# Optimization experiments

Measured on AMD Instinct MI355X. Metric: run time of the kernel, lower is better.

## Reference

```python
import jax, jax.numpy as jnp
import numpy as np

B, T, D, F, E, K = 2, 1024, 1024, 2048, 8, 2

def setup_inputs() -> dict:
    key = jax.random.key(0)
    ks = jax.random.split(key, 9)
    s = 0.02
    return {
        "states": jax.random.normal(ks[0], (B, T, D), dtype=jnp.float32),
        "Wg": jax.random.normal(ks[1], (D, E), dtype=jnp.float32) * s,
        "W_in": jax.random.normal(ks[2], (E, D, F), dtype=jnp.float32) * s,
        "b_in": jnp.zeros((E, F), dtype=jnp.float32),
        "W_scale": jax.random.normal(ks[3], (E, D, F), dtype=jnp.float32) * s,
        "b_scale": jnp.zeros((E, F), dtype=jnp.float32),
        "W_out": jax.random.normal(ks[4], (E, F, D), dtype=jnp.float32) * s,
        "b_out": jnp.zeros((E, D), dtype=jnp.float32),
        "num_selected": K,
    }

def reference(states, Wg, W_in, b_in, W_scale, b_scale, W_out, b_out, num_selected):
    b, t, d = states.shape
    x = states.reshape(-1, d)                      # [N, D]
    n = x.shape[0]
    # router: softmax over experts, then top-k + renormalize
    probs = jax.nn.softmax(x @ Wg, axis=-1)        # [N, E]
    topw, topi = jax.lax.top_k(probs, num_selected)  # [N, K]
    topw = topw / topw.sum(axis=-1, keepdims=True)
    # dense combine weights [N, E]: zero except selected experts
    w_full = jnp.zeros_like(probs).at[jnp.arange(n)[:, None], topi].set(topw)
    # gated-GELU expert MLPs, batched over experts
    h = jnp.einsum('nd,edf->enf', x, W_in) + b_in[:, None, :]       # [E, N, F]
    s = jnp.einsum('nd,edf->enf', x, W_scale) + b_scale[:, None, :]
    inner = jax.nn.gelu(h, approximate=False) * s                    # exact GELU (torch default)
    y = jnp.einsum('enf,efd->end', inner, W_out) + b_out[:, None, :]  # [E, N, D]
    out = jnp.einsum('end,ne->nd', y, w_full)                         # weighted combine
    return out.reshape(b, t, d)
```

## Files before the change

kernel.cpp:

```cpp
#include <hip/hip_runtime.h>
#include <hip/hip_bf16.h>
#include <math.h>

#define N_TOK 2048
#define DIM   1024
#define FF    2048
#define NEXP  8
#define NSLOT (N_TOK * 2)

typedef __attribute__((ext_vector_type(8))) short short8;
typedef __attribute__((ext_vector_type(4))) float f32x4;
typedef _Float16 half_t;
typedef __attribute__((ext_vector_type(4))) _Float16 h16x4;

__device__ __forceinline__ unsigned short f2bf(float f) {
    unsigned int u = __float_as_uint(f);
    u += 0x7FFFu + ((u >> 16) & 1u);
    return (unsigned short)(u >> 16);
}

#define GLOAD_LDS16(g, l) \
    __builtin_amdgcn_global_load_lds((const __attribute__((address_space(1))) unsigned int*)(g), \
                                     (__attribute__((address_space(3))) unsigned int*)(l), 16, 0, 0)

__global__ __launch_bounds__(256) void k_router(const float* __restrict__ x,
        const float* __restrict__ Wg, int* __restrict__ hdr,
        int* __restrict__ tok_e, float* __restrict__ tok_w) {
    int wave = threadIdx.x >> 6, lane = threadIdx.x & 63;
    int t = blockIdx.x * 4 + wave;
    float acc[NEXP];
#pragma unroll
    for (int e = 0; e < NEXP; ++e) acc[e] = 0.f;
    const float* xr = x + (size_t)t * DIM;
    for (int d = lane; d < DIM; d += 64) {
        float xv = xr[d];
        const float* wr = Wg + d * NEXP;
#pragma unroll
        for (int e = 0; e < NEXP; ++e) acc[e] += xv * wr[e];
    }
#pragma unroll
    for (int off = 32; off > 0; off >>= 1) {
#pragma unroll
        for (int e = 0; e < NEXP; ++e) acc[e] += __shfl_down(acc[e], off);
    }
    if (lane == 0) {
        int e0 = 0;
#pragma unroll
        for (int e = 1; e < NEXP; ++e) if (acc[e] > acc[e0]) e0 = e;
        int e1 = -1;
#pragma unroll
        for (int e = 0; e < NEXP; ++e) {
            if (e == e0) continue;
            if (e1 < 0 || acc[e] > acc[e1]) e1 = e;
        }
        float w0 = 1.f / (1.f + expf(acc[e1] - acc[e0]));
        tok_e[2 * t] = e0; tok_e[2 * t + 1] = e1;
        tok_w[2 * t] = w0; tok_w[2 * t + 1] = 1.f - w0;
        atomicAdd(&hdr[e0], 1);
        atomicAdd(&hdr[e1], 1);
    }
}

__global__ void k_scan(int* hdr) {
    if (threadIdx.x == 0 && blockIdx.x == 0) {
        int s = 0;
        for (int e = 0; e < NEXP; ++e) {
            hdr[16 + e] = s;
            hdr[8 + e]  = s;
            s += hdr[e];
        }
        hdr[24] = s;
    }
}

__global__ __launch_bounds__(256) void k_assign(const float* __restrict__ x,
        int* __restrict__ hdr, const int* __restrict__ tok_e,
        int* __restrict__ tok_slot, unsigned short* __restrict__ xg) {
    __shared__ int sh[2];
    int t = blockIdx.x;
    if (threadIdx.x == 0) {
        int e0 = tok_e[2 * t], e1 = tok_e[2 * t + 1];
        int p0 = atomicAdd(&hdr[8 + e0], 1);
        int p1 = atomicAdd(&hdr[8 + e1], 1);
        tok_slot[2 * t] = p0; tok_slot[2 * t + 1] = p1;
        sh[0] = p0; sh[1] = p1;
    }
    __syncthreads();
    int s0 = sh[0], s1 = sh[1];
    const float4* xr = (const float4*)(x + (size_t)t * DIM);
    float4 v = xr[threadIdx.x];
    ushort4 b;
    b.x = f2bf(v.x); b.y = f2bf(v.y); b.z = f2bf(v.z); b.w = f2bf(v.w);
    ((ushort4*)(xg + (size_t)s0 * DIM))[threadIdx.x] = b;
    ((ushort4*)(xg + (size_t)s1 * DIM))[threadIdx.x] = b;
}

__global__ __launch_bounds__(256) void k_cvt(
        const float* __restrict__ s0, const float* __restrict__ s1,
        const float* __restrict__ s2, unsigned short* __restrict__ d0,
        unsigned short* __restrict__ d1, unsigned short* __restrict__ d2) {
    int bz = blockIdx.y;
    int which = bz >> 3, e = bz & 7;
    int R = (which == 2) ? FF : DIM;
    int C = (which == 2) ? DIM : FF;
    const float* S = ((which == 0) ? s0 : (which == 1) ? s1 : s2) + (size_t)e * DIM * FF;
    unsigned short* D = ((which == 0) ? d0 : (which == 1) ? d1 : d2) + (size_t)e * DIM * FF;
    int tilesx = C >> 6;
    int tx = blockIdx.x % tilesx, ty = blockIdx.x / tilesx;
    int c0 = tx * 64, r0 = ty * 128;
    __shared__ unsigned short sh[64][132];
    int t = threadIdx.x;
    int rl = t >> 4, cl = (t & 15) * 4;
#pragma unroll
    for (int p = 0; p < 8; ++p) {
        int r = p * 16 + rl;
        float4 v = *(const float4*)(S + (size_t)(r0 + r) * C + c0 + cl);
        sh[cl + 0][r] = f2bf(v.x);
        sh[cl + 1][r] = f2bf(v.y);
        sh[cl + 2][r] = f2bf(v.z);
        sh[cl + 3][r] = f2bf(v.w);
    }
    __syncthreads();
    int ol = t >> 4, wl = (t & 15) * 8;
#pragma unroll
    for (int p = 0; p < 4; ++p) {
        int oc = p * 16 + ol;
        uint2 lo = *(const uint2*)&sh[oc][wl];
        uint2 hi = *(const uint2*)&sh[oc][wl + 4];
        uint4 v = make_uint4(lo.x, lo.y, hi.x, hi.y);
        *(uint4*)(D + (size_t)(c0 + oc) * R + r0 + wl) = v;
    }
}

__global__ __launch_bounds__(256, 4) void k_expert_hs(
        const unsigned short* __restrict__ xg,
        const unsigned short* __restrict__ Wth,
        const unsigned short* __restrict__ Wts,
        const float* __restrict__ b_in, const float* __restrict__ b_sc,
        const int* __restrict__ hdr, unsigned short* __restrict__ inner) {
    int e = blockIdx.z;
    int cnt = hdr[e];
    int mtile = blockIdx.y;
    if (mtile * 128 >= cnt) return;
    int base = hdr[16 + e];
    int f0 = blockIdx.x * 64;

    __shared__ unsigned short As[2 * 128 * 32];
    __shared__ unsigned short Bh[2 * 64 * 32];
    __shared__ unsigned short Bs[2 * 64 * 32];

    int tid = threadIdx.x;
    int wave = tid >> 6, lane = tid & 63;
    int lr = lane & 15, lq = lane >> 4;
    int wm = (wave >> 1) * 64, wf = (wave & 1) * 32;

    f32x4 acch[4][2], accs[4][2];
#pragma unroll
    for (int mi = 0; mi < 4; ++mi)
#pragma unroll
        for (int fi = 0; fi < 2; ++fi) {
            acch[mi][fi] = (f32x4){0.f, 0.f, 0.f, 0.f};
            accs[mi][fi] = (f32x4){0.f, 0.f, 0.f, 0.f};
        }

    int swzc = (lane & 3) ^ ((lane >> 3) & 3);
    int goff = (lane >> 2) * DIM + swzc * 8;
    int rdo = lr * 32 + (lq ^ ((lr >> 1) & 3)) * 8;

    const unsigned short* Abase = xg  + (size_t)(base + mtile * 128) * DIM + goff;
    const unsigned short* Hbase = Wth + ((size_t)e * FF + f0) * DIM + goff;
    const unsigned short* Sbase = Wts + ((size_t)e * FF + f0) * DIM + goff;
    int pa0 = wave * 16, pa1 = 64 + wave * 16, pb = wave * 16;

    GLOAD_LDS16(Abase + (size_t)pa0 * DIM, &As[pa0 * 32]);
    GLOAD_LDS16(Abase + (size_t)pa1 * DIM, &As[pa1 * 32]);
    GLOAD_LDS16(Hbase + (size_t)pb * DIM, &Bh[pb * 32]);
    GLOAD_LDS16(Sbase + (size_t)pb * DIM, &Bs[pb * 32]);
    __syncthreads();

    const int NSTEP = DIM / 32;
    for (int t = 0; t < NSTEP; ++t) {
        int coA = (t & 1) * (128 * 32), coB = (t & 1) * (64 * 32);
        if (t + 1 < NSTEP) {
            int noA = ((t & 1) ^ 1) * (128 * 32), noB = ((t & 1) ^ 1) * (64 * 32);
            int k1 = (t + 1) * 32;
            GLOAD_LDS16(Abase + (size_t)pa0 * DIM + k1, &As[noA + pa0 * 32]);
            GLOAD_LDS16(Abase + (size_t)pa1 * DIM + k1, &As[noA + pa1 * 32]);
            GLOAD_LDS16(Hbase + (size_t)pb * DIM + k1, &Bh[noB + pb * 32]);
            GLOAD_LDS16(Sbase + (size_t)pb * DIM + k1, &Bs[noB + pb * 32]);
        }

        short8 af[4], bhf[2], bsf[2];
#pragma unroll
        for (int mi = 0; mi < 4; ++mi)
            af[mi] = *(const short8*)&As[coA + (wm + mi * 16) * 32 + rdo];
#pragma unroll
        for (int fi = 0; fi < 2; ++fi) {
            bhf[fi] = *(const short8*)&Bh[coB + (wf + fi * 16) * 32 + rdo];
            bsf[fi] = *(const short8*)&Bs[coB + (wf + fi * 16) * 32 + rdo];
        }
#pragma unroll
        for (int mi = 0; mi < 4; ++mi)
#pragma unroll
            for (int fi = 0; fi < 2; ++fi) {
                acch[mi][fi] = __builtin_amdgcn_mfma_f32_16x16x32_bf16(
                    af[mi], bhf[fi], acch[mi][fi], 0, 0, 0);
                accs[mi][fi] = __builtin_amdgcn_mfma_f32_16x16x32_bf16(
                    af[mi], bsf[fi], accs[mi][fi], 0, 0, 0);
            }
        __syncthreads();
    }

#pragma unroll
    for (int fi = 0; fi < 2; ++fi) {
        int f = f0 + wf + fi * 16 + lr;
        float bi = b_in[e * FF + f];
        float bs2 = b_sc[e * FF + f];
#pragma unroll
        for (int mi = 0; mi < 4; ++mi) {
#pragma unroll
            for (int r = 0; r < 4; ++r) {
                int rl = wm + mi * 16 + lq * 4 + r;
                int grow = mtile * 128 + rl;
                if (grow < cnt) {
                    float h = acch[mi][fi][r] + bi;
                    float s = accs[mi][fi][r] + bs2;
                    float g = 0.5f * h * (1.f + erff(h * 0.70710678f));
                    inner[(size_t)(base + grow) * FF + f] = f2bf(g * s);
                }
            }
        }
    }
}

__global__ __launch_bounds__(256, 4) void k_expert_out(
        const unsigned short* __restrict__ inner,
        const unsigned short* __restrict__ Wto,
        const int* __restrict__ hdr, half_t* __restrict__ pbuf) {
    int e = blockIdx.z & 7;
    int ks = blockIdx.z >> 3;
    int cnt = hdr[e];
    int mtile = blockIdx.y;
    if (mtile * 128 >= cnt) return;
    int base = hdr[16 + e];
    int d0 = blockIdx.x * 128;

    __shared__ unsigned short As[2 * 128 * 32];
    __shared__ unsigned short Bt[2 * 128 * 32];

    int tid = threadIdx.x;
    int wave = tid >> 6, lane = tid & 63;
    int lr = lane & 15, lq = lane >> 4;
    int wm = (wave >> 1) * 64, wn = (wave & 1) * 64;

    f32x4 acc[4][4];
#pragma unroll
    for (int mi = 0; mi < 4; ++mi)
#pragma unroll
        for (int ni = 0; ni < 4; ++ni) acc[mi][ni] = (f32x4){0.f, 0.f, 0.f, 0.f};

    int swzc = (lane & 3) ^ ((lane >> 3) & 3);
    int goff = (lane >> 2) * FF + swzc * 8;
    int rdo = lr * 32 + (lq ^ ((lr >> 1) & 3)) * 8;

    const unsigned short* Abase = inner + (size_t)(base + mtile * 128) * FF + goff;
    const unsigned short* Bbase = Wto + ((size_t)e * DIM + d0) * FF + goff;
    int pa0 = wave * 16, pa1 = 64 + wave * 16;

    int kbeg = ks * (FF / 2);

    GLOAD_LDS16(Abase + (size_t)pa0 * FF + kbeg, &As[pa0 * 32]);
    GLOAD_LDS16(Abase + (size_t)pa1 * FF + kbeg, &As[pa1 * 32]);
    GLOAD_LDS16(Bbase + (size_t)pa0 * FF + kbeg, &Bt[pa0 * 32]);
    GLOAD_LDS16(Bbase + (size_t)pa1 * FF + kbeg, &Bt[pa1 * 32]);
    __syncthreads();

    const int NSTEP = (FF / 2) / 32;
    for (int t = 0; t < NSTEP; ++t) {
        int co = (t & 1) * (128 * 32);
        if (t + 1 < NSTEP) {
            int no = ((t & 1) ^ 1) * (128 * 32);
            int k1 = kbeg + (t + 1) * 32;
            GLOAD_LDS16(Abase + (size_t)pa0 * FF + k1, &As[no + pa0 * 32]);
            GLOAD_LDS16(Abase + (size_t)pa1 * FF + k1, &As[no + pa1 * 32]);
            GLOAD_LDS16(Bbase + (size_t)pa0 * FF + k1, &Bt[no + pa0 * 32]);
            GLOAD_LDS16(Bbase + (size_t)pa1 * FF + k1, &Bt[no + pa1 * 32]);
        }

        short8 af[4], bfm[4];
#pragma unroll
        for (int mi = 0; mi < 4; ++mi)
            af[mi] = *(const short8*)&As[co + (wm + mi * 16) * 32 + rdo];
#pragma unroll
        for (int ni = 0; ni < 4; ++ni)
            bfm[ni] = *(const short8*)&Bt[co + (wn + ni * 16) * 32 + rdo];
#pragma unroll
        for (int mi = 0; mi < 4; ++mi)
#pragma unroll
            for (int ni = 0; ni < 4; ++ni)
                acc[mi][ni] = __builtin_amdgcn_mfma_f32_16x16x32_bf16(
                    af[mi], bfm[ni], acc[mi][ni], 0, 0, 0);
        __syncthreads();
    }

    half_t* P = pbuf + (size_t)ks * NSLOT * DIM;
#pragma unroll
    for (int ni = 0; ni < 4; ++ni) {
        int d = d0 + wn + ni * 16 + lr;
#pragma unroll
        for (int mi = 0; mi < 4; ++mi) {
#pragma unroll
            for (int r = 0; r < 4; ++r) {
                int rl = wm + mi * 16 + lq * 4 + r;
                int grow = mtile * 128 + rl;
                if (grow < cnt)
                    P[(size_t)(base + grow) * DIM + d] = (half_t)acc[mi][ni][r];
            }
        }
    }
}

__global__ __launch_bounds__(256) void k_combine(const half_t* __restrict__ pbuf,
        const int* __restrict__ tok_slot, const int* __restrict__ tok_e,
        const float* __restrict__ tok_w, const float* __restrict__ b_out,
        float* __restrict__ out) {
    int t = blockIdx.x;
    int d = threadIdx.x * 4;
    int s0 = tok_slot[2 * t], s1 = tok_slot[2 * t + 1];
    int e0 = tok_e[2 * t], e1 = tok_e[2 * t + 1];
    float w0 = tok_w[2 * t], w1 = tok_w[2 * t + 1];
    const half_t* pA = pbuf;
    const half_t* pB = pbuf + (size_t)NSLOT * DIM;
    h16x4 a0 = *(const h16x4*)&pA[(size_t)s0 * DIM + d];
    h16x4 a1 = *(const h16x4*)&pB[(size_t)s0 * DIM + d];
    h16x4 c0 = *(const h16x4*)&pA[(size_t)s1 * DIM + d];
    h16x4 c1 = *(const h16x4*)&pB[(size_t)s1 * DIM + d];
    float4 b0 = *(const float4*)&b_out[e0 * DIM + d];
    float4 b1 = *(const float4*)&b_out[e1 * DIM + d];
    float4 r;
    r.x = w0 * ((float)a0.x + (float)a1.x + b0.x) + w1 * ((float)c0.x + (float)c1.x + b1.x);
    r.y = w0 * ((float)a0.y + (float)a1.y + b0.y) + w1 * ((float)c0.y + (float)c1.y + b1.y);
    r.z = w0 * ((float)a0.z + (float)a1.z + b0.z) + w1 * ((float)c0.z + (float)c1.z + b1.z);
    r.w = w0 * ((float)a0.w + (float)a1.w + b0.w) + w1 * ((float)c0.w + (float)c1.w + b1.w);
    *(float4*)&out[(size_t)t * DIM + d] = r;
}

extern "C" void kernel_launch(void* const* d_in, const int* in_sizes, int n_in,
                              void* d_out, int out_size, void* d_ws, size_t ws_size,
                              hipStream_t stream) {
    (void)in_sizes; (void)n_in; (void)out_size; (void)ws_size;
    const float* x    = (const float*)d_in[0];
    const float* Wg   = (const float*)d_in[1];
    const float* Win  = (const float*)d_in[2];
    const float* b_in = (const float*)d_in[3];
    const float* Wsc  = (const float*)d_in[4];
    const float* b_sc = (const float*)d_in[5];
    const float* Wout = (const float*)d_in[6];
    const float* b_out= (const float*)d_in[7];
    float* out = (float*)d_out;

    char* ws = (char*)d_ws;
    int*   hdr      = (int*)ws;
    int*   tok_e    = (int*)(ws + 256);
    float* tok_w    = (float*)(ws + 16640);
    int*   tok_slot = (int*)(ws + 33024);
    unsigned short* xg    = (unsigned short*)(ws + 65792);
    unsigned short* inner = (unsigned short*)(ws + 65792 + 8388608);
    half_t* pbuf = (half_t*)(ws + 65792 + 8388608 + 16777216);
    unsigned short* wt_h = (unsigned short*)(ws + 65792 + 8388608 + 16777216 + 16777216);
    unsigned short* wt_s = wt_h + (size_t)NEXP * FF * DIM;
    unsigned short* wt_o = wt_s + (size_t)NEXP * FF * DIM;

    hipMemsetAsync(hdr, 0, 256, stream);
    k_cvt<<<dim3(256, 24), dim3(256), 0, stream>>>(Win, Wsc, Wout, wt_h, wt_s, wt_o);
    k_router<<<dim3(N_TOK / 4), dim3(256), 0, stream>>>(x, Wg, hdr, tok_e, tok_w);
    k_scan<<<dim3(1), dim3(64), 0, stream>>>(hdr);
    k_assign<<<dim3(N_TOK), dim3(256), 0, stream>>>(x, hdr, tok_e, tok_slot, xg);
    k_expert_hs<<<dim3(FF / 64, 16, NEXP), dim3(256), 0, stream>>>(xg, wt_h, wt_s, b_in, b_sc, hdr, inner);
    k_expert_out<<<dim3(DIM / 128, 16, NEXP * 2), dim3(256), 0, stream>>>(inner, wt_o, hdr, pbuf);
    k_combine<<<dim3(N_TOK), dim3(256), 0, stream>>>(pbuf, tok_slot, tok_e, tok_w, b_out, out);
}
```

Baseline: 446.0 us.

## Fuse weight conversion, routing and token scatter into one prep kernel

Merges the weight transpose/convert kernel, the router, the scan and the token assignment into a single launch. When the workspace is large enough, each expert gets a fixed slab of N_TOK slots, so the router can assign slots with atomics directly and scatter bf16 token rows itself, dropping the scan and assign launches. The conversion tiles are also enlarged to 256 rows per block. This removes launches and serialization between small kernels, at the cost of a much larger workspace and sparser slot layout, and it falls back to the old path when the workspace is small.

Measured after the change: 437.3 us. 2.0% less time.

```diff
diff --git a/kernel.cpp b/kernel.cpp
--- a/kernel.cpp
+++ b/kernel.cpp
@@ -7,6 +7,7 @@
 #define FF    2048
 #define NEXP  8
 #define NSLOT (N_TOK * 2)
+#define NCVT  3072
 
 typedef __attribute__((ext_vector_type(8))) short short8;
 typedef __attribute__((ext_vector_type(4))) float f32x4;
@@ -23,15 +24,64 @@
     __builtin_amdgcn_global_load_lds((const __attribute__((address_space(1))) unsigned int*)(g), \
                                      (__attribute__((address_space(3))) unsigned int*)(l), 16, 0, 0)
 
-__global__ __launch_bounds__(256) void k_router(const float* __restrict__ x,
-        const float* __restrict__ Wg, int* __restrict__ hdr,
-        int* __restrict__ tok_e, float* __restrict__ tok_w) {
-    int wave = threadIdx.x >> 6, lane = threadIdx.x & 63;
-    int t = blockIdx.x * 4 + wave;
+__global__ __launch_bounds__(256) void k_prep(
+        const float* __restrict__ x, const float* __restrict__ Wg,
+        const float* __restrict__ Win, const float* __restrict__ Wsc,
+        const float* __restrict__ Wout,
+        unsigned short* __restrict__ wt_h, unsigned short* __restrict__ wt_s,
+        unsigned short* __restrict__ wt_o,
+        int* __restrict__ hdr, int* __restrict__ tok_e,
+        float* __restrict__ tok_w, int* __restrict__ tok_slot,
+        unsigned short* __restrict__ xg, int mode) {
+    __shared__ unsigned short sh[64][260];
+    int gid = blockIdx.x;
+    int t = threadIdx.x;
+
+    if (gid < NCVT) {
+        int bz = gid >> 7;
+        int which = bz >> 3, e = bz & 7;
+        int R = (which == 2) ? FF : DIM;
+        int C = (which == 2) ? DIM : FF;
+        const float* S = ((which == 0) ? Win : (which == 1) ? Wsc : Wout)
+                         + (size_t)e * DIM * FF;
+        unsigned short* D = ((which == 0) ? wt_h : (which == 1) ? wt_s : wt_o)
+                            + (size_t)e * DIM * FF;
+        int local = gid & 127;
+        int tilesx = C >> 6;
+        int tx = local % tilesx, ty = local / tilesx;
+        int c0 = tx * 64, r0 = ty * 256;
+        int rl = t >> 4, cl = (t & 15) * 4;
+#pragma unroll
+        for (int p = 0; p < 16; ++p) {
+            int r = p * 16 + rl;
+            float4 v = *(const float4*)(S + (size_t)(r0 + r) * C + c0 + cl);
+            sh[cl + 0][r] = f2bf(v.x);
+            sh[cl + 1][r] = f2bf(v.y);
+            sh[cl + 2][r] = f2bf(v.z);
+            sh[cl + 3][r] = f2bf(v.w);
+        }
+        __syncthreads();
+        int ol = t >> 5, wl = (t & 31) * 8;
+#pragma unroll
+        for (int q = 0; q < 8; ++q) {
+            int oc = q * 8 + ol;
+            uint2 lo = *(const uint2*)&sh[oc][wl];
+            uint2 hi = *(const uint2*)&sh[oc][wl + 4];
+            *(uint4*)(D + (size_t)(c0 + oc) * R + r0 + wl) =
+                make_uint4(lo.x, lo.y, hi.x, hi.y);
+        }
+        return;
+    }
+
+    int rblk = gid - NCVT;
+    int wave = t >> 6, lane = t & 63;
+    int tok = rblk * 4 + wave;
+    if (mode && gid == NCVT && t < NEXP) hdr[16 + t] = t * N_TOK;
+
     float acc[NEXP];
 #pragma unroll
     for (int e = 0; e < NEXP; ++e) acc[e] = 0.f;
-    const float* xr = x + (size_t)t * DIM;
+    const float* xr = x + (size_t)tok * DIM;
     for (int d = lane; d < DIM; d += 64) {
         float xv = xr[d];
         const float* wr = Wg + d * NEXP;
@@ -43,6 +93,7 @@
 #pragma unroll
         for (int e = 0; e < NEXP; ++e) acc[e] += __shfl_down(acc[e], off);
     }
+    int s0 = 0, s1 = 0;
     if (lane == 0) {
         int e0 = 0;
 #pragma unroll
@@ -54,10 +105,29 @@
             if (e1 < 0 || acc[e] > acc[e1]) e1 = e;
         }
         float w0 = 1.f / (1.f + expf(acc[e1] - acc[e0]));
-        tok_e[2 * t] = e0; tok_e[2 * t + 1] = e1;
-        tok_w[2 * t] = w0; tok_w[2 * t + 1] = 1.f - w0;
-        atomicAdd(&hdr[e0], 1);
-        atomicAdd(&hdr[e1], 1);
+        tok_e[2 * tok] = e0; tok_e[2 * tok + 1] = e1;
+        tok_w[2 * tok] = w0; tok_w[2 * tok + 1] = 1.f - w0;
+        if (mode) {
+            int p0 = atomicAdd(&hdr[e0], 1);
+            int p1 = atomicAdd(&hdr[e1], 1);
+            s0 = e0 * N_TOK + p0; s1 = e1 * N_TOK + p1;
+            tok_slot[2 * tok] = s0; tok_slot[2 * tok + 1] = s1;
+        } else {
+            atomicAdd(&hdr[e0], 1);
+            atomicAdd(&hdr[e1], 1);
+        }
+    }
+    if (mode) {
+        s0 = __shfl(s0, 0); s1 = __shfl(s1, 0);
+        const float4* xv4 = (const float4*)xr;
+#pragma unroll
+        for (int j = 0; j < 4; ++j) {
+            float4 v = xv4[lane + j * 64];
+            ushort4 b;
+            b.x = f2bf(v.x); b.y = f2bf(v.y); b.z = f2bf(v.z); b.w = f2bf(v.w);
+            ((ushort4*)(xg + (size_t)s0 * DIM))[lane + j * 64] = b;
+            ((ushort4*)(xg + (size_t)s1 * DIM))[lane + j * 64] = b;
+        }
     }
 }
 
@@ -93,43 +163,6 @@
     b.x = f2bf(v.x); b.y = f2bf(v.y); b.z = f2bf(v.z); b.w = f2bf(v.w);
     ((ushort4*)(xg + (size_t)s0 * DIM))[threadIdx.x] = b;
     ((ushort4*)(xg + (size_t)s1 * DIM))[threadIdx.x] = b;
-}
-
-__global__ __launch_bounds__(256) void k_cvt(
-        const float* __restrict__ s0, const float* __restrict__ s1,
-        const float* __restrict__ s2, unsigned short* __restrict__ d0,
-        unsigned short* __restrict__ d1, unsigned short* __restrict__ d2) {
-    int bz = blockIdx.y;
-    int which = bz >> 3, e = bz & 7;
-    int R = (which == 2) ? FF : DIM;
-    int C = (which == 2) ? DIM : FF;
-    const float* S = ((which == 0) ? s0 : (which == 1) ? s1 : s2) + (size_t)e * DIM * FF;
-    unsigned short* D = ((which == 0) ? d0 : (which == 1) ? d1 : d2) + (size_t)e * DIM * FF;
-    int tilesx = C >> 6;
-    int tx = blockIdx.x % tilesx, ty = blockIdx.x / tilesx;
-    int c0 = tx * 64, r0 = ty * 128;
-    __shared__ unsigned short sh[64][132];
-    int t = threadIdx.x;
-    int rl = t >> 4, cl = (t & 15) * 4;
-#pragma unroll
-    for (int p = 0; p < 8; ++p) {
-        int r = p * 16 + rl;
-        float4 v = *(const float4*)(S + (size_t)(r0 + r) * C + c0 + cl);
-        sh[cl + 0][r] = f2bf(v.x);
-        sh[cl + 1][r] = f2bf(v.y);
-        sh[cl + 2][r] = f2bf(v.z);
-        sh[cl + 3][r] = f2bf(v.w);
-    }
-    __syncthreads();
-    int ol = t >> 4, wl = (t & 15) * 8;
-#pragma unroll
-    for (int p = 0; p < 4; ++p) {
-        int oc = p * 16 + ol;
-        uint2 lo = *(const uint2*)&sh[oc][wl];
-        uint2 hi = *(const uint2*)&sh[oc][wl + 4];
-        uint4 v = make_uint4(lo.x, lo.y, hi.x, hi.y);
-        *(uint4*)(D + (size_t)(c0 + oc) * R + r0 + wl) = v;
-    }
 }
 
 __global__ __launch_bounds__(256, 4) void k_expert_hs(
@@ -236,7 +269,7 @@
 __global__ __launch_bounds__(256, 4) void k_expert_out(
         const unsigned short* __restrict__ inner,
         const unsigned short* __restrict__ Wto,
-        const int* __restrict__ hdr, half_t* __restrict__ pbuf) {
+        const int* __restrict__ hdr, half_t* __restrict__ pbuf, int pstride) {
     int e = blockIdx.z & 7;
     int ks = blockIdx.z >> 3;
     int cnt = hdr[e];
@@ -303,7 +336,7 @@
         __syncthreads();
     }
 
-    half_t* P = pbuf + (size_t)ks * NSLOT * DIM;
+    half_t* P = pbuf + (size_t)ks * pstride * DIM;
 #pragma unroll
     for (int ni = 0; ni < 4; ++ni) {
         int d = d0 + wn + ni * 16 + lr;
@@ -323,14 +356,14 @@
 __global__ __launch_bounds__(256) void k_combine(const half_t* __restrict__ pbuf,
         const int* __restrict__ tok_slot, const int* __restrict__ tok_e,
         const float* __restrict__ tok_w, const float* __restrict__ b_out,
-        float* __restrict__ out) {
+        float* __restrict__ out, int pstride) {
     int t = blockIdx.x;
     int d = threadIdx.x * 4;
     int s0 = tok_slot[2 * t], s1 = tok_slot[2 * t + 1];
     int e0 = tok_e[2 * t], e1 = tok_e[2 * t + 1];
     float w0 = tok_w[2 * t], w1 = tok_w[2 * t + 1];
     const half_t* pA = pbuf;
-    const half_t* pB = pbuf + (size_t)NSLOT * DIM;
+    const half_t* pB = pbuf + (size_t)pstride * DIM;
     h16x4 a0 = *(const h16x4*)&pA[(size_t)s0 * DIM + d];
     h16x4 a1 = *(const h16x4*)&pB[(size_t)s0 * DIM + d];
     h16x4 c0 = *(const h16x4*)&pA[(size_t)s1 * DIM + d];
@@ -348,7 +381,7 @@
 extern "C" void kernel_launch(void* const* d_in, const int* in_sizes, int n_in,
                               void* d_out, int out_size, void* d_ws, size_t ws_size,
                               hipStream_t stream) {
-    (void)in_sizes; (void)n_in; (void)out_size; (void)ws_size;
+    (void)in_sizes; (void)n_in; (void)out_size;
     const float* x    = (const float*)d_in[0];
     const float* Wg   = (const float*)d_in[1];
     const float* Win  = (const float*)d_in[2];
@@ -364,19 +397,43 @@
     int*   tok_e    = (int*)(ws + 256);
     float* tok_w    = (float*)(ws + 16640);
     int*   tok_slot = (int*)(ws + 33024);
-    unsigned short* xg    = (unsigned short*)(ws + 65792);
-    unsigned short* inner = (unsigned short*)(ws + 65792 + 8388608);
-    half_t* pbuf = (half_t*)(ws + 65792 + 8388608 + 16777216);
-    unsigned short* wt_h = (unsigned short*)(ws + 65792 + 8388608 + 16777216 + 16777216);
-    unsigned short* wt_s = wt_h + (size_t)NEXP * FF * DIM;
-    unsigned short* wt_o = wt_s + (size_t)NEXP * FF * DIM;
+
+    const size_t BIG_NEED = 65792ULL + (32ULL + 64 + 64 + 96) * 1024 * 1024;
+    int big = (ws_size >= BIG_NEED) ? 1 : 0;
+
+    unsigned short *xg, *inner, *wt_h, *wt_s, *wt_o;
+    half_t* pbuf;
+    int slab;
+    if (big) {
+        xg    = (unsigned short*)(ws + 65792);
+        inner = (unsigned short*)(ws + 65792 + 33554432);
+        pbuf  = (half_t*)(ws + 65792 + 33554432 + 67108864);
+        wt_h  = (unsigned short*)(ws + 65792 + 33554432 + 67108864 + 67108864);
+        wt_s  = wt_h + (size_t)NEXP * FF * DIM;
+        wt_o  = wt_s + (size_t)NEXP * FF * DIM;
+        slab  = NEXP * N_TOK;
+    } else {
+        xg    = (unsigned short*)(ws + 65792);
+        inner = (unsigned short*)(ws + 65792 + 8388608);
+        pbuf  = (half_t*)(ws + 65792 + 8388608 + 16777216);
+        wt_h  = (unsigned short*)(ws + 65792 + 8388608 + 16777216 + 16777216);
+        wt_s  = wt_h + (size_t)NEXP * FF * DIM;
+        wt_o  = wt_s + (size_t)NEXP * FF * DIM;
+        slab  = NSLOT;
+    }
 
     hipMemsetAsync(hdr, 0, 256, stream);
-    k_cvt<<<dim3(256, 24), dim3(256), 0, stream>>>(Win, Wsc, Wout, wt_h, wt_s, wt_o);
-    k_router<<<dim3(N_TOK / 4), dim3(256), 0, stream>>>(x, Wg, hdr, tok_e, tok_w);
-    k_scan<<<dim3(1), dim3(64), 0, stream>>>(hdr);
-    k_assign<<<dim3(N_TOK), dim3(256), 0, stream>>>(x, hdr, tok_e, tok_slot, xg);
-    k_expert_hs<<<dim3(FF / 64, 16, NEXP), dim3(256), 0, stream>>>(xg, wt_h, wt_s, b_in, b_sc, hdr, inner);
-    k_expert_out<<<dim3(DIM / 128, 16, NEXP * 2), dim3(256), 0, stream>>>(inner, wt_o, hdr, pbuf);
-    k_combine<<<dim3(N_TOK), dim3(256), 0, stream>>>(pbuf, tok_slot, tok_e, tok_w, b_out, out);
-}
+    k_prep<<<dim3(NCVT + N_TOK / 4), dim3(256), 0, stream>>>(
+        x, Wg, Win, Wsc, Wout, wt_h, wt_s, wt_o,
+        hdr, tok_e, tok_w, tok_slot, xg, big);
+    if (!big) {
+        k_scan<<<dim3(1), dim3(64), 0, stream>>>(hdr);
+        k_assign<<<dim3(N_TOK), dim3(256), 0, stream>>>(x, hdr, tok_e, tok_slot, xg);
+    }
+    k_expert_hs<<<dim3(FF / 64, 16, NEXP), dim3(256), 0, stream>>>(
+        xg, wt_h, wt_s, b_in, b_sc, hdr, inner);
+    k_expert_out<<<dim3(DIM / 128, 16, NEXP * 2), dim3(256), 0, stream>>>(
+        inner, wt_o, hdr, pbuf, slab);
+    k_combine<<<dim3(N_TOK), dim3(256), 0, stream>>>(
+        pbuf, tok_slot, tok_e, tok_w, b_out, out, slab);
+}
```
